# Optimization experiments

Hardware: AMD Instinct MI355X
Metric: run time of the kernel (lower is better)

Reference implementation:

```python
import jax, jax.numpy as jnp
import numpy as np

B, N, K, H = 8, 1024, 16, 4
EMB = 1024

def lrelu(x):
    return jnp.where(x >= 0, x, 0.2 * x)

def bn(x, g, b):
    # eval-mode BatchNorm with running_mean=0, running_var=1
    inv = 1.0 / np.sqrt(1.0 + 1e-5)
    shape = (1, -1) + (1,) * (x.ndim - 2)
    return x * (g * inv).reshape(shape) + b.reshape(shape)

def conv1x1(x, w):
    # 1x1 conv == channel matmul; x: (B,C,...), w: (O,C)
    return jnp.einsum('bc...,oc->bo...', x, w)

def knn_idx(x, k):
    # x: (B,C,N); negative squared pairwise distance, top-k largest = nearest
    inner = -2.0 * jnp.einsum('bcn,bcm->bnm', x, x)
    xx = jnp.sum(x * x, axis=1)                      # (B,N)
    pd = -xx[:, :, None] - inner - xx[:, None, :]
    return jax.lax.top_k(pd, k)[1]                   # (B,N,k)

def graph_feature(x, idx):
    b = x.shape[0]
    xt = jnp.transpose(x, (0, 2, 1))                 # (B,N,C)
    nbr = xt[jnp.arange(b)[:, None, None], idx]      # (B,N,K,C) gather
    ctr = jnp.broadcast_to(xt[:, :, None, :], nbr.shape)
    f = jnp.concatenate([nbr - ctr, ctr], axis=-1)   # (B,N,K,2C)
    return jnp.transpose(f, (0, 3, 1, 2))            # (B,2C,N,K)

def mak(x, y, w0, g0, b0, wm, gm, bm, w1, go, bo, ws, gs, bs, out_ch, in_ch):
    # Multi-head adaptive kernel: generate per-point (out,in,H) weights from y, apply to x
    Bc, _, Nc, Kc = x.shape
    y = lrelu(bn(conv1x1(y, w0), g0, b0))
    y = lrelu(bn(conv1x1(y, wm), gm, bm))
    y = conv1x1(y, w1)                               # (B, out*in*H, N, K)
    w = jnp.transpose(y, (0, 2, 3, 1)).reshape(Bc, Nc, Kc, out_ch, in_ch, H)
    xt = jnp.transpose(x, (0, 2, 3, 1))              # (B,N,K,in)
    # per-head matmul then sum over heads == single einsum over i and h
    out = jnp.einsum('bnkoih,bnki->bonk', w, xt)
    out = bn(out, go, bo)
    idt = bn(conv1x1(x, ws), gs, bs)                 # shortcut (in != out)
    return lrelu(out + idt)


def setup_inputs() -> dict:
    ks = jax.random.split(jax.random.key(0), 48)
    it = iter(range(48))
    def nrm(shape, fan):
        return jax.random.normal(ks[next(it)], shape, jnp.float32) / np.sqrt(fan)
    def gam(c):
        return jax.random.uniform(ks[next(it)], (c,), jnp.float32, 0.5, 1.5)
    def bet(c):
        return 0.1 * jax.random.normal(ks[next(it)], (c,), jnp.float32)
    d = {}
    d['x'] = jax.random.normal(ks[next(it)], (B, 3, N), jnp.float32)
    def mak_params(p, feat_c):
        d[p + '_w0'] = nrm((64, feat_c), feat_c); d[p + '_g0'] = gam(64); d[p + '_b0'] = bet(64)
        d[p + '_wm'] = nrm((64, 64), 64); d[p + '_gm'] = gam(64); d[p + '_bm'] = bet(64)
        d[p + '_w1'] = nrm((64 * 6 * H, 64), 64)
        d[p + '_go'] = gam(64); d[p + '_bo'] = bet(64)
        d[p + '_ws'] = nrm((64, 6), 6); d[p + '_gs'] = gam(64); d[p + '_bs'] = bet(64)
    mak_params('m1', 6)
    mak_params('m2', 128)
    d['w3'] = nrm((128, 128), 128); d['g3'] = gam(128); d['b3'] = bet(128)
    d['w4'] = nrm((256, 256), 256); d['g4'] = gam(256); d['b4'] = bet(256)
    d['w5'] = nrm((EMB, 512), 512); d['g5'] = gam(EMB); d['b5'] = bet(EMB)
    d['wl1'] = nrm((512, 2 * EMB), 2 * EMB); d['bn4_g'] = gam(512); d['bn4_b'] = bet(512)
    d['wl2'] = nrm((256, 512), 512); d['bl2'] = bet(256); d['bn5_g'] = gam(256); d['bn5_b'] = bet(256)
    d['wl3'] = nrm((49, 256), 256); d['bl3'] = bet(49)
    return d


def reference(x, m1_w0, m1_g0, m1_b0, m1_wm, m1_gm, m1_bm, m1_w1, m1_go, m1_bo, m1_ws, m1_gs, m1_bs, m2_w0, m2_g0, m2_b0, m2_wm, m2_gm, m2_bm, m2_w1, m2_go, m2_bo, m2_ws, m2_gs, m2_bs, w3, g3, b3, w4, g4, b4, w5, g5, b5, wl1, bn4_g, bn4_b, wl2, bl2, bn5_g, bn5_b, wl3, bl3):
    idx = knn_idx(x, K)                              # common_idx from points
    geo = graph_feature(x, idx)                      # (B,6,N,K); feat_x == geo_x at stage 1
    h = mak(geo, geo, m1_w0, m1_g0, m1_b0, m1_wm, m1_gm, m1_bm, m1_w1, m1_go, m1_bo, m1_ws, m1_gs, m1_bs, 64, 6)
    x1 = h.max(axis=-1)                              # (B,64,N)
    feat2 = graph_feature(x1, idx)                   # (B,128,N,K)
    h = mak(geo, feat2, m2_w0, m2_g0, m2_b0, m2_wm, m2_gm, m2_bm, m2_w1, m2_go, m2_bo, m2_ws, m2_gs, m2_bs, 64, 6)
    x2 = h.max(axis=-1)                              # (B,64,N)
    x3 = lrelu(bn(conv1x1(graph_feature(x2, idx), w3), g3, b3)).max(axis=-1)   # (B,128,N)
    x4 = lrelu(bn(conv1x1(graph_feature(x3, idx), w4), g4, b4)).max(axis=-1)   # (B,256,N)
    xc = jnp.concatenate([x1, x2, x3, x4], axis=1)   # (B,512,N)
    x5 = lrelu(bn(conv1x1(xc, w5), g5, b5))          # (B,EMB,N)
    xp = jnp.concatenate([x5.max(axis=-1), x5.mean(axis=-1)], axis=1)  # (B,2*EMB)
    xf = lrelu(bn(xp @ wl1.T, bn4_g, bn4_b))
    xf = lrelu(bn(xf @ wl2.T + bl2, bn5_g, bn5_b))
    return xf @ wl3.T + bl3                           # (B,49)
```

## Files before the change

### kernel.cpp

```cpp
#include <hip/hip_runtime.h>
#include <math.h>

#define BB 8
#define NN 1024
#define KK 16
#define NKP (NN*KK)
#define BN_INV 0.99999500003749981f

typedef unsigned short u16;
typedef __attribute__((ext_vector_type(8))) short short8;
typedef __attribute__((ext_vector_type(4))) float f32x4;

#define MFMA16(a,b,c) __builtin_amdgcn_mfma_f32_16x16x32_bf16(a,b,c,0,0,0)

__device__ __forceinline__ float lrelu(float v) { return v >= 0.f ? v : 0.2f * v; }

__device__ __forceinline__ u16 f2bf(float f) {
  union { float f; unsigned u; } v; v.f = f;
  unsigned r = v.u + 0x7fff + ((v.u >> 16) & 1);
  return (u16)(r >> 16);
}
__device__ __forceinline__ float bf2f(u16 s) {
  union { unsigned u; float f; } v; v.u = ((unsigned)s) << 16;
  return v.f;
}

constexpr size_t OFF_IDX   = 0;
constexpr size_t OFF_X1P   = 524288;
constexpr size_t OFF_X2P   = 1572864;
constexpr size_t OFF_X3P   = 2621440;
constexpr size_t OFF_X4P   = 4718592;
constexpr size_t OFF_PMAX  = 8912896;
constexpr size_t OFF_PSUM  = 9437184;
constexpr size_t OFF_XP    = 9961472;
constexpr size_t OFF_XF1   = 10027008;
constexpr size_t OFF_XF2   = 10043392;
constexpr size_t OFF_M1W0  = 10051584;
constexpr size_t OFF_M1WM  = 10055680;
constexpr size_t OFF_M1W1S = 10063872;
constexpr size_t OFF_M2W0  = 10117120;
constexpr size_t OFF_M2WM  = 10133504;
constexpr size_t OFF_M2W1S = 10141696;
constexpr size_t OFF_W3S   = 10194944;
constexpr size_t OFF_W4S   = 10227712;
constexpr size_t OFF_W5    = 10358784;
constexpr size_t OFF_WL1T  = 11407360;
constexpr size_t OFF_WL2T  = 15601664;
constexpr size_t OFF_WL3T  = 16125952;
constexpr size_t OFF_UV3   = 16177152;
constexpr size_t OFF_UV4   = 20371456;

struct SSeg { const float* w; const float* g; u16* dst; int O; int C; int cpl2; int ch; int stk; int start; };
struct SArgs { SSeg seg[7]; int total; };

__global__ __launch_bounds__(256) void prep_scale_bf16(SArgs a) {
  const int tid = blockIdx.x * 256 + threadIdx.x;
  if (tid >= a.total) return;
  int s = 0;
  #pragma unroll
  for (int i = 1; i < 7; ++i) if (tid >= a.seg[i].start) s = i;
  const SSeg sg = a.seg[s];
  const int e = tid - sg.start;
  const int o2 = e >> sg.cpl2;
  const int c = e & ((1 << sg.cpl2) - 1);
  float v = 0.f;
  if (sg.stk) {
    const int half = sg.O >> 1;
    const int o = o2 & (half - 1);
    const int CIN = 2 * sg.C;
    const float wd = sg.w[o * CIN + c];
    v = (o2 < half) ? wd : (sg.w[o * CIN + sg.C + c] - wd);
    v *= sg.g[o] * BN_INV;
  } else if (c < sg.C) {
    v = sg.w[o2 * sg.C + c];
    if (sg.ch && c >= sg.ch) v -= sg.w[o2 * sg.C + c - sg.ch];
    v *= sg.g[o2] * BN_INV;
  }
  sg.dst[(size_t)(c >> 5) * (sg.O * 32) + o2 * 32 + (c & 31)] = f2bf(v);
}

__global__ __launch_bounds__(256) void prep_w1s_bf16(
    const float* __restrict__ w1a, const float* __restrict__ wsa,
    const float* __restrict__ goa, const float* __restrict__ gsa,
    const float* __restrict__ w1b, const float* __restrict__ wsb,
    const float* __restrict__ gob, const float* __restrict__ gsb,
    u16* __restrict__ dsta, u16* __restrict__ dstb) {
  const int tid = blockIdx.x * 256 + threadIdx.x;
  if (tid >= 64 * 416) return;
  const float* w1 = blockIdx.y ? w1b : w1a;
  const float* wsm = blockIdx.y ? wsb : wsa;
  const float* go = blockIdx.y ? gob : goa;
  const float* gs = blockIdx.y ? gsb : gsa;
  u16* dst = blockIdx.y ? dstb : dsta;
  const int o = tid / 416, ci = tid - o * 416;
  float v = 0.f;
  if (ci < 384) {
    const int ii = ci >> 6, ch = ci & 63;
    const int base = (o * 24 + ii * 4) * 64 + ch;
    v = go[o] * BN_INV * (w1[base] + w1[base + 64] + w1[base + 128] + w1[base + 192]);
  } else if (ci < 390) {
    v = gs[o] * BN_INV * wsm[o * 6 + (ci - 384)];
  }
  dst[(size_t)(ci >> 5) * 2048 + o * 32 + (ci & 31)] = f2bf(v);
}

struct TSeg { const float* w; const float* g; float* dst; int O; int C; int start; };
struct TArgs3 { TSeg seg[3]; int total; };

__global__ __launch_bounds__(256) void prep_transpose_f32(TArgs3 a) {
  const int tid = blockIdx.x * 256 + threadIdx.x;
  if (tid >= a.total) return;
  int s = 0;
  #pragma unroll
  for (int i = 1; i < 3; ++i) if (tid >= a.seg[i].start) s = i;
  const TSeg sg = a.seg[s];
  const int e = tid - sg.start;
  const int c = e / sg.O;
  const int o = e - c * sg.O;
  float v = sg.w[o * sg.C + c];
  if (sg.g) v *= sg.g[o] * BN_INV;
  sg.dst[e] = v;
}

__global__ __launch_bounds__(256) void knn_kernel(const float* __restrict__ x, int* __restrict__ idxout) {
  const int wid  = (blockIdx.x * blockDim.x + threadIdx.x) >> 6;
  const int lane = threadIdx.x & 63;
  const int b = wid >> 10;
  const int n = wid & (NN - 1);
  const float* xb = x + b * 3 * NN;
  const float x0n = xb[n], x1n = xb[NN + n], x2n = xb[2 * NN + n];
  const float xxn = x0n * x0n + x1n * x1n + x2n * x2n;
  float pd[16];
  #pragma unroll
  for (int j = 0; j < 16; ++j) {
    const int m = j * 64 + lane;
    const float x0 = xb[m], x1 = xb[NN + m], x2 = xb[2 * NN + m];
    const float dot = x0n * x0 + x1n * x1 + x2n * x2;
    const float xxm = x0 * x0 + x1 * x1 + x2 * x2;
    pd[j] = 2.f * dot - xxn - xxm;
  }
  for (int r = 0; r < 16; ++r) {
    float bv = pd[0]; int bj = 0;
    #pragma unroll
    for (int j = 1; j < 16; ++j) if (pd[j] > bv) { bv = pd[j]; bj = j; }
    int bm = bj * 64 + lane;
    #pragma unroll
    for (int off = 32; off > 0; off >>= 1) {
      const float ov = __shfl_down(bv, off);
      const int   om = __shfl_down(bm, off);
      if (ov > bv || (ov == bv && om < bm)) { bv = ov; bm = om; }
    }
    bm = __shfl(bm, 0);
    if (lane == 0) idxout[wid * KK + r] = bm;
    const int  cj   = bm >> 6;
    const bool mine = (bm & 63) == lane;
    #pragma unroll
    for (int j = 0; j < 16; ++j) if (mine && j == cj) pd[j] = -INFINITY;
  }
}

__device__ __forceinline__ short8 bfrag64(const u16* T, int pl, int quad, int c0) {
  const int pos = ((c0 >> 3) + quad) ^ (pl & 7);
  return *(const short8*)(T + pl * 64 + pos * 8);
}
__device__ __forceinline__ void writeD64(u16* T, int pl, int quad, const f32x4 a,
                                         const float* __restrict__ bias, int obase) {
  union { ushort4 v; u16 s[4]; } pk;
  #pragma unroll
  for (int r = 0; r < 4; ++r) pk.s[r] = f2bf(lrelu(a[r] + bias[obase + quad * 4 + r]));
  const int g = (obase + quad * 4) >> 3;
  const int pos = g ^ (pl & 7);
  *(ushort4*)(T + pl * 64 + pos * 8 + (quad & 1) * 4) = pk.v;
}

template<int CIN_Y>
__global__ __launch_bounds__(256) void mak_mfma(
    const float* __restrict__ x, const int* __restrict__ idxb, const u16* __restrict__ srcp,
    const u16* __restrict__ w0b, const float* __restrict__ b0v,
    const u16* __restrict__ wmb, const float* __restrict__ bmv,
    const u16* __restrict__ w1s, const float* __restrict__ bov, const float* __restrict__ bsv,
    u16* __restrict__ Xoutp) {
  __shared__ __align__(16) u16 Y0s[64 * 64];
  __shared__ __align__(16) u16 YMs[64 * 64];

  const int t = threadIdx.x;
  const int b = blockIdx.z;
  const int p0 = blockIdx.x * 64;
  const int w = t >> 6, l = t & 63;
  const int quad = l >> 4, l15 = l & 15;
  const int pl = w * 16 + l15;
  const int cq8 = quad * 8;
  const int nvtx = blockIdx.x * 4 + w;

  const int nbr = idxb[b * NKP + p0 + pl] & (NN - 1);

  const float* xb = x + b * 3 * NN;
  float ge[6];
  #pragma unroll
  for (int i = 0; i < 3; ++i) {
    const float fc = xb[i * NN + nvtx];
    ge[i]     = xb[i * NN + nbr] - fc;
    ge[3 + i] = fc;
  }
  union { short8 v; u16 s[8]; } bg;
  bg.v = (short8)(short)0;
  if (quad == 0) {
    #pragma unroll
    for (int j = 0; j < 6; ++j) bg.s[j] = f2bf(ge[j]);
  }

  f32x4 acc[4];
  #pragma unroll
  for (int i = 0; i < 4; ++i) acc[i] = (f32x4)0.f;

  if constexpr (CIN_Y == 6) {
    #pragma unroll
    for (int at = 0; at < 4; ++at) {
      const short8 af = *(const short8*)(w0b + (size_t)(at * 16 + l15) * 32 + cq8);
      acc[at] = MFMA16(af, bg.v, acc[at]);
    }
  } else {
    short8 bf[4];
    #pragma unroll
    for (int k = 0; k < 2; ++k)
      bf[k] = *(const short8*)(srcp + (size_t)(b * NN + nbr) * 64 + k * 32 + cq8);
    #pragma unroll
    for (int k = 2; k < 4; ++k)
      bf[k] = *(const short8*)(srcp + (size_t)(b * NN + nvtx) * 64 + (k - 2) * 32 + cq8);
    #pragma unroll
    for (int k = 0; k < 4; ++k) {
      #pragma unroll
      for (int at = 0; at < 4; ++at) {
        const short8 af = *(const short8*)(w0b + (size_t)(k * 64 + at * 16 + l15) * 32 + cq8);
        acc[at] = MFMA16(af, bf[k], acc[at]);
      }
    }
  }
  #pragma unroll
  for (int at = 0; at < 4; ++at) writeD64(Y0s, pl, quad, acc[at], b0v, at * 16);

  #pragma unroll
  for (int i = 0; i < 4; ++i) acc[i] = (f32x4)0.f;
  #pragma unroll
  for (int kc = 0; kc < 2; ++kc) {
    const short8 bf = bfrag64(Y0s, pl, quad, kc * 32);
    #pragma unroll
    for (int at = 0; at < 4; ++at) {
      const short8 af = *(const short8*)(wmb + (size_t)(kc * 64 + at * 16 + l15) * 32 + cq8);
      acc[at] = MFMA16(af, bf, acc[at]);
    }
  }
  #pragma unroll
  for (int at = 0; at < 4; ++at) writeD64(YMs, pl, quad, acc[at], bmv, at * 16);

  short8 bf3[2];
  #pragma unroll
  for (int kc = 0; kc < 2; ++kc) bf3[kc] = bfrag64(YMs, pl, quad, kc * 32);

  #pragma unroll
  for (int i = 0; i < 4; ++i) acc[i] = (f32x4)0.f;
  #pragma unroll
  for (int ii = 0; ii < 6; ++ii) {
    f32x4 tacc[4];
    #pragma unroll
    for (int i = 0; i < 4; ++i) tacc[i] = (f32x4)0.f;
    #pragma unroll
    for (int kc = 0; kc < 2; ++kc) {
      #pragma unroll
      for (int at = 0; at < 4; ++at) {
        const short8 af = *(const short8*)(w1s + (size_t)((ii * 2 + kc) * 64 + at * 16 + l15) * 32 + cq8);
        tacc[at] = MFMA16(af, bf3[kc], tacc[at]);
      }
    }
    const float g = ge[ii];
    #pragma unroll
    for (int at = 0; at < 4; ++at) acc[at] += g * tacc[at];
  }
  #pragma unroll
  for (int at = 0; at < 4; ++at) {
    const short8 af = *(const short8*)(w1s + (size_t)(12 * 64 + at * 16 + l15) * 32 + cq8);
    acc[at] = MFMA16(af, bg.v, acc[at]);
  }

  u16* orow = Xoutp + (size_t)(b * NN + nvtx) * 64;
  #pragma unroll
  for (int at = 0; at < 4; ++at) {
    union { ushort4 v; u16 s[4]; } pk;
    #pragma unroll
    for (int r = 0; r < 4; ++r) {
      const int o = at * 16 + quad * 4 + r;
      float v = lrelu(acc[at][r] + bov[o] + bsv[o]);
      v = fmaxf(v, __shfl_xor(v, 1));
      v = fmaxf(v, __shfl_xor(v, 2));
      v = fmaxf(v, __shfl_xor(v, 4));
      v = fmaxf(v, __shfl_xor(v, 8));
      pk.s[r] = f2bf(v);
    }
    if (l15 == 0) *(ushort4*)(orow + at * 16 + quad * 4) = pk.v;
  }
}

template<int CH, int COUT2>
__global__ __launch_bounds__(256) void dense_uv(
    const u16* __restrict__ srcp, const u16* __restrict__ w2,
    const float* __restrict__ bias, u16* __restrict__ UV) {
  constexpr int COUT = COUT2 / 2;
  constexpr int NCH = CH / 32;
  const int t = threadIdx.x;
  const int b = blockIdx.z;
  const int n0 = blockIdx.x * 64;
  const int w = t >> 6, l = t & 63;
  const int quad = l >> 4, l15 = l & 15;
  const int cq8 = quad * 8;
  const int ow0 = blockIdx.y * 256 + w * 64;

  f32x4 acc[4][4];
  #pragma unroll
  for (int i = 0; i < 4; ++i)
    #pragma unroll
    for (int j = 0; j < 4; ++j) acc[i][j] = (f32x4)0.f;

  #pragma unroll
  for (int k = 0; k < NCH; ++k) {
    short8 bfr[4];
    #pragma unroll
    for (int pg = 0; pg < 4; ++pg) {
      const int n = n0 + pg * 16 + l15;
      bfr[pg] = *(const short8*)(srcp + (size_t)(b * NN + n) * CH + k * 32 + cq8);
    }
    #pragma unroll
    for (int at = 0; at < 4; ++at) {
      const short8 af = *(const short8*)(w2 + ((size_t)(k * COUT2 + ow0 + at * 16 + l15)) * 32 + cq8);
      #pragma unroll
      for (int pg = 0; pg < 4; ++pg) acc[at][pg] = MFMA16(af, bfr[pg], acc[at][pg]);
    }
  }

  #pragma unroll
  for (int at = 0; at < 4; ++at) {
    const int o0 = ow0 + at * 16 + quad * 4;
    const bool isv = (o0 >= COUT);
    float bb[4];
    #pragma unroll
    for (int r = 0; r < 4; ++r) bb[r] = isv ? bias[o0 + r - COUT] : 0.f;
    #pragma unroll
    for (int pg = 0; pg < 4; ++pg) {
      const int n = n0 + pg * 16 + l15;
      union { ushort4 v; u16 s[4]; } pk;
      #pragma unroll
      for (int r = 0; r < 4; ++r) pk.s[r] = f2bf(acc[at][pg][r] + bb[r]);
      *(ushort4*)(UV + (size_t)(b * NN + n) * COUT2 + o0) = pk.v;
    }
  }
}

__device__ __forceinline__ float4 ubf4(ushort4 q) {
  float4 f;
  f.x = bf2f(q.x); f.y = bf2f(q.y); f.z = bf2f(q.z); f.w = bf2f(q.w);
  return f;
}

template<int COUT>
__global__ __launch_bounds__(256) void gather_max(
    const u16* __restrict__ UV, const int* __restrict__ idxb,
    u16* __restrict__ Xoutp) {
  constexpr int CG = COUT / 4;
  const int tid = blockIdx.x * 256 + threadIdx.x;
  const int cg = tid & (CG - 1);
  const int P = tid / CG;
  const int b = P >> 10;
  const int n = P & (NN - 1);

  const float4 vv = ubf4(*(const ushort4*)(UV + (size_t)P * (2 * COUT) + COUT + 4 * cg));
  const int4* ip = (const int4*)(idxb + (size_t)b * NKP + n * 16);
  float4 m = {-INFINITY, -INFINITY, -INFINITY, -INFINITY};
  #pragma unroll
  for (int kq = 0; kq < 4; ++kq) {
    const int4 iv = ip[kq];
    const int mr[4] = { iv.x & (NN - 1), iv.y & (NN - 1), iv.z & (NN - 1), iv.w & (NN - 1) };
    ushort4 uq[4];
    #pragma unroll
    for (int j = 0; j < 4; ++j)
      uq[j] = *(const ushort4*)(UV + (size_t)(b * NN + mr[j]) * (2 * COUT) + 4 * cg);
    #pragma unroll
    for (int j = 0; j < 4; ++j) {
      const float4 uu = ubf4(uq[j]);
      float4 s;
      s.x = uu.x + vv.x; s.y = uu.y + vv.y; s.z = uu.z + vv.z; s.w = uu.w + vv.w;
      m.x = fmaxf(m.x, fmaxf(s.x, 0.2f * s.x));
      m.y = fmaxf(m.y, fmaxf(s.y, 0.2f * s.y));
      m.z = fmaxf(m.z, fmaxf(s.z, 0.2f * s.z));
      m.w = fmaxf(m.w, fmaxf(s.w, 0.2f * s.w));
    }
  }
  union { ushort4 v; u16 s[4]; } pk;
  pk.s[0] = f2bf(m.x); pk.s[1] = f2bf(m.y); pk.s[2] = f2bf(m.z); pk.s[3] = f2bf(m.w);
  *(ushort4*)(Xoutp + (size_t)P * COUT + 4 * cg) = pk.v;
}

__global__ __launch_bounds__(256) void conv5_mfma(
    const u16* __restrict__ X1P, const u16* __restrict__ X2P,
    const u16* __restrict__ X3P, const u16* __restrict__ X4P,
    const u16* __restrict__ w5b, const float* __restrict__ b5,
    float* __restrict__ PMAX, float* __restrict__ PSUM) {
  const int t = threadIdx.x;
  const int b = blockIdx.z;
  const int n0 = blockIdx.x * 64;
  const int w = t >> 6, l = t & 63;
  const int quad = l >> 4, l15 = l & 15;
  const int cq8 = quad * 8;
  const int ow0 = blockIdx.y * 256 + w * 64;

  f32x4 acc[4][4];
  #pragma unroll
  for (int i = 0; i < 4; ++i)
    #pragma unroll
    for (int j = 0; j < 4; ++j) acc[i][j] = (f32x4)0.f;

  #pragma unroll 4
  for (int k = 0; k < 16; ++k) {
    const int c = k * 32 + cq8;
    short8 bfr[4];
    #pragma unroll
    for (int pg = 0; pg < 4; ++pg) {
      const int n = n0 + pg * 16 + l15;
      const u16* src; int cc;
      if (c < 64)       { src = X1P + (size_t)(b * NN + n) * 64;  cc = c; }
      else if (c < 128) { src = X2P + (size_t)(b * NN + n) * 64;  cc = c - 64; }
      else if (c < 256) { src = X3P + (size_t)(b * NN + n) * 128; cc = c - 128; }
      else              { src = X4P + (size_t)(b * NN + n) * 256; cc = c - 256; }
      bfr[pg] = *(const short8*)(src + cc);
    }
    #pragma unroll
    for (int at = 0; at < 4; ++at) {
      const short8 af = *(const short8*)(w5b + ((size_t)(k * 1024 + ow0 + at * 16 + l15)) * 32 + cq8);
      #pragma unroll
      for (int pg = 0; pg < 4; ++pg) acc[at][pg] = MFMA16(af, bfr[pg], acc[at][pg]);
    }
  }

  #pragma unroll
  for (int at = 0; at < 4; ++at) {
    f32x4 pmx, psm;
    #pragma unroll
    for (int r = 0; r < 4; ++r) {
      const float bb = b5[ow0 + at * 16 + quad * 4 + r];
      float m = -INFINITY, s = 0.f;
      #pragma unroll
      for (int pg = 0; pg < 4; ++pg) {
        const float v = lrelu(acc[at][pg][r] + bb);
        m = fmaxf(m, v); s += v;
      }
      #pragma unroll
      for (int msk = 1; msk < 16; msk <<= 1) {
        m = fmaxf(m, __shfl_xor(m, msk));
        s += __shfl_xor(s, msk);
      }
      pmx[r] = m; psm[r] = s;
    }
    if (l15 == 0) {
      float* dm = PMAX + (size_t)(b * 16 + blockIdx.x) * 1024 + ow0 + at * 16 + quad * 4;
      float* ds = PSUM + (size_t)(b * 16 + blockIdx.x) * 1024 + ow0 + at * 16 + quad * 4;
      *(f32x4*)dm = pmx;
      *(f32x4*)ds = psm;
    }
  }
}

__global__ __launch_bounds__(256) void reduce5(const float* __restrict__ PMAX, const float* __restrict__ PSUM,
                                               float* __restrict__ XPg) {
  const int tid = blockIdx.x * 256 + threadIdx.x;
  const int b = tid >> 10, o = tid & 1023;
  float m = -INFINITY, s = 0.f;
  for (int pt = 0; pt < 16; ++pt) {
    m = fmaxf(m, PMAX[(size_t)(b * 16 + pt) * 1024 + o]);
    s += PSUM[(size_t)(b * 16 + pt) * 1024 + o];
  }
  XPg[b * 2048 + o] = m;
  XPg[b * 2048 + 1024 + o] = s * (1.f / 1024.f);
}

__global__ __launch_bounds__(256) void fc1_kernel(const float* __restrict__ XPg, const float* __restrict__ wl1t,
                                                  const float* __restrict__ bn4_b, float* __restrict__ XF1) {
  __shared__ float red[64 * 5];
  const int t = threadIdx.x;
  const int b = blockIdx.y;
  const int o = blockIdx.x * 64 + (t & 63);
  const int cq = t >> 6;
  const float* xp = XPg + b * 2048;
  float acc = 0.f;
  for (int c = cq * 512; c < cq * 512 + 512; ++c) acc = fmaf(wl1t[c * 512 + o], xp[c], acc);
  red[(t & 63) * 5 + cq] = acc;
  __syncthreads();
  if (t < 64) {
    const int oo = blockIdx.x * 64 + t;
    const float v = red[t * 5] + red[t * 5 + 1] + red[t * 5 + 2] + red[t * 5 + 3] + bn4_b[oo];
    XF1[b * 512 + oo] = lrelu(v);
  }
}

__global__ __launch_bounds__(256) void fc2_kernel(const float* __restrict__ XF1, const float* __restrict__ wl2t,
                                                  const float* __restrict__ bl2, const float* __restrict__ bn5_g,
                                                  const float* __restrict__ bn5_b, float* __restrict__ XF2) {
  __shared__ float red[64 * 5];
  const int t = threadIdx.x;
  const int b = blockIdx.y;
  const int o = blockIdx.x * 64 + (t & 63);
  const int cq = t >> 6;
  const float* xf = XF1 + b * 512;
  float acc = 0.f;
  for (int c = cq * 128; c < cq * 128 + 128; ++c) acc = fmaf(wl2t[c * 256 + o], xf[c], acc);
  red[(t & 63) * 5 + cq] = acc;
  __syncthreads();
  if (t < 64) {
    const int oo = blockIdx.x * 64 + t;
    const float bias = bl2[oo] * (bn5_g[oo] * BN_INV) + bn5_b[oo];
    const float v = red[t * 5] + red[t * 5 + 1] + red[t * 5 + 2] + red[t * 5 + 3] + bias;
    XF2[b * 256 + oo] = lrelu(v);
  }
}

__global__ __launch_bounds__(256) void fc3_kernel(const float* __restrict__ XF2, const float* __restrict__ wl3t,
                                                  const float* __restrict__ bl3, float* __restrict__ out) {
  __shared__ float red[64 * 5];
  const int t = threadIdx.x;
  const int b = blockIdx.y;
  const int ol = t & 63;
  const int cq = t >> 6;
  const float* xf = XF2 + b * 256;
  float acc = 0.f;
  if (ol < 49) for (int c = cq * 64; c < cq * 64 + 64; ++c) acc = fmaf(wl3t[c * 49 + ol], xf[c], acc);
  red[ol * 5 + cq] = acc;
  __syncthreads();
  if (t < 49) out[b * 49 + t] = red[t * 5] + red[t * 5 + 1] + red[t * 5 + 2] + red[t * 5 + 3] + bl3[t];
}

extern "C" void kernel_launch(void* const* d_in, const int* in_sizes, int n_in,
                              void* d_out, int out_size, void* d_ws, size_t ws_size,
                              hipStream_t stream) {
  (void)in_sizes; (void)n_in; (void)out_size; (void)ws_size;
  const float* x     = (const float*)d_in[0];
  const float* m1_w0 = (const float*)d_in[1];
  const float* m1_g0 = (const float*)d_in[2];
  const float* m1_b0 = (const float*)d_in[3];
  const float* m1_wm = (const float*)d_in[4];
  const float* m1_gm = (const float*)d_in[5];
  const float* m1_bm = (const float*)d_in[6];
  const float* m1_w1 = (const float*)d_in[7];
  const float* m1_go = (const float*)d_in[8];
  const float* m1_bo = (const float*)d_in[9];
  const float* m1_ws = (const float*)d_in[10];
  const float* m1_gs = (const float*)d_in[11];
  const float* m1_bs = (const float*)d_in[12];
  const float* m2_w0 = (const float*)d_in[13];
  const float* m2_g0 = (const float*)d_in[14];
  const float* m2_b0 = (const float*)d_in[15];
  const float* m2_wm = (const float*)d_in[16];
  const float* m2_gm = (const float*)d_in[17];
  const float* m2_bm = (const float*)d_in[18];
  const float* m2_w1 = (const float*)d_in[19];
  const float* m2_go = (const float*)d_in[20];
  const float* m2_bo = (const float*)d_in[21];
  const float* m2_ws = (const float*)d_in[22];
  const float* m2_gs = (const float*)d_in[23];
  const float* m2_bs = (const float*)d_in[24];
  const float* w3    = (const float*)d_in[25];
  const float* g3    = (const float*)d_in[26];
  const float* b3    = (const float*)d_in[27];
  const float* w4    = (const float*)d_in[28];
  const float* g4    = (const float*)d_in[29];
  const float* b4    = (const float*)d_in[30];
  const float* w5    = (const float*)d_in[31];
  const float* g5    = (const float*)d_in[32];
  const float* b5    = (const float*)d_in[33];
  const float* wl1   = (const float*)d_in[34];
  const float* bn4_g = (const float*)d_in[35];
  const float* bn4_b = (const float*)d_in[36];
  const float* wl2   = (const float*)d_in[37];
  const float* bl2   = (const float*)d_in[38];
  const float* bn5_g = (const float*)d_in[39];
  const float* bn5_b = (const float*)d_in[40];
  const float* wl3   = (const float*)d_in[41];
  const float* bl3   = (const float*)d_in[42];

  char* wsb = (char*)d_ws;
  int*  IDX  = (int*)(wsb + OFF_IDX);
  u16*  X1P  = (u16*)(wsb + OFF_X1P);
  u16*  X2P  = (u16*)(wsb + OFF_X2P);
  u16*  X3P  = (u16*)(wsb + OFF_X3P);
  u16*  X4P  = (u16*)(wsb + OFF_X4P);
  float* PMAX = (float*)(wsb + OFF_PMAX);
  float* PSUM = (float*)(wsb + OFF_PSUM);
  float* XPg  = (float*)(wsb + OFF_XP);
  float* XF1  = (float*)(wsb + OFF_XF1);
  float* XF2  = (float*)(wsb + OFF_XF2);
  u16*  M1W0 = (u16*)(wsb + OFF_M1W0);
  u16*  M1WM = (u16*)(wsb + OFF_M1WM);
  u16*  M1W1S = (u16*)(wsb + OFF_M1W1S);
  u16*  M2W0 = (u16*)(wsb + OFF_M2W0);
  u16*  M2WM = (u16*)(wsb + OFF_M2WM);
  u16*  M2W1S = (u16*)(wsb + OFF_M2W1S);
  u16*  W3S  = (u16*)(wsb + OFF_W3S);
  u16*  W4S  = (u16*)(wsb + OFF_W4S);
  u16*  W5B  = (u16*)(wsb + OFF_W5);
  float* WL1T = (float*)(wsb + OFF_WL1T);
  float* WL2T = (float*)(wsb + OFF_WL2T);
  float* WL3T = (float*)(wsb + OFF_WL3T);
  u16*  UV3  = (u16*)(wsb + OFF_UV3);
  u16*  UV4  = (u16*)(wsb + OFF_UV4);

  SArgs sa; int st = 0;
  auto sset = [&](int i, const float* w, const float* g, u16* dst, int O, int C, int cpl2, int ch, int stk) {
    sa.seg[i].w = w; sa.seg[i].g = g; sa.seg[i].dst = dst; sa.seg[i].O = O; sa.seg[i].C = C;
    sa.seg[i].cpl2 = cpl2; sa.seg[i].ch = ch; sa.seg[i].stk = stk; sa.seg[i].start = st;
    st += O << cpl2;
  };
  sset(0, m1_w0, m1_g0, M1W0, 64, 6, 5, 0, 0);
  sset(1, m1_wm, m1_gm, M1WM, 64, 64, 6, 0, 0);
  sset(2, m2_w0, m2_g0, M2W0, 64, 128, 7, 64, 0);
  sset(3, m2_wm, m2_gm, M2WM, 64, 64, 6, 0, 0);
  sset(4, w3, g3, W3S, 256, 64, 6, 0, 1);
  sset(5, w4, g4, W4S, 512, 128, 7, 0, 1);
  sset(6, w5, g5, W5B, 1024, 512, 9, 0, 0);
  sa.total = st;

  TArgs3 ta; int tt = 0;
  auto tset = [&](int i, const float* w, const float* g, float* dst, int O, int C) {
    ta.seg[i].w = w; ta.seg[i].g = g; ta.seg[i].dst = dst; ta.seg[i].O = O; ta.seg[i].C = C;
    ta.seg[i].start = tt; tt += O * C;
  };
  tset(0, wl1, bn4_g, WL1T, 512, 2048);
  tset(1, wl2, bn5_g, WL2T, 256, 512);
  tset(2, wl3, nullptr, WL3T, 49, 256);
  ta.total = tt;

  hipLaunchKernelGGL(prep_scale_bf16, dim3((sa.total + 255) / 256), dim3(256), 0, stream, sa);
  hipLaunchKernelGGL(prep_w1s_bf16, dim3(104, 2), dim3(256), 0, stream,
                     m1_w1, m1_ws, m1_go, m1_gs, m2_w1, m2_ws, m2_go, m2_gs, M1W1S, M2W1S);
  hipLaunchKernelGGL(prep_transpose_f32, dim3((ta.total + 255) / 256), dim3(256), 0, stream, ta);

  hipLaunchKernelGGL(knn_kernel, dim3(2048), dim3(256), 0, stream, x, IDX);

  hipLaunchKernelGGL((mak_mfma<6>), dim3(256, 1, BB), dim3(256), 0, stream,
                     x, IDX, (const u16*)nullptr, M1W0, m1_b0, M1WM, m1_bm, M1W1S, m1_bo, m1_bs, X1P);
  hipLaunchKernelGGL((mak_mfma<128>), dim3(256, 1, BB), dim3(256), 0, stream,
                     x, IDX, X1P, M2W0, m2_b0, M2WM, m2_bm, M2W1S, m2_bo, m2_bs, X2P);

  hipLaunchKernelGGL((dense_uv<64, 256>), dim3(16, 1, BB), dim3(256), 0, stream, X2P, W3S, b3, UV3);
  hipLaunchKernelGGL((gather_max<128>), dim3(1024), dim3(256), 0, stream, UV3, IDX, X3P);

  hipLaunchKernelGGL((dense_uv<128, 512>), dim3(16, 2, BB), dim3(256), 0, stream, X3P, W4S, b4, UV4);
  hipLaunchKernelGGL((gather_max<256>), dim3(2048), dim3(256), 0, stream, UV4, IDX, X4P);

  hipLaunchKernelGGL(conv5_mfma, dim3(16, 4, BB), dim3(256), 0, stream,
                     X1P, X2P, X3P, X4P, W5B, b5, PMAX, PSUM);
  hipLaunchKernelGGL(reduce5, dim3(32), dim3(256), 0, stream, PMAX, PSUM, XPg);

  hipLaunchKernelGGL(fc1_kernel, dim3(8, BB), dim3(256), 0, stream, XPg, WL1T, bn4_b, XF1);
  hipLaunchKernelGGL(fc2_kernel, dim3(4, BB), dim3(256), 0, stream, XF1, WL2T, bl2, bn5_g, bn5_b, XF2);
  hipLaunchKernelGGL(fc3_kernel, dim3(1, BB), dim3(256), 0, stream, XF2, WL3T, bl3, (float*)d_out);
}
```

Baseline: 386.8 us.

## Factor MAK first conv into per-point U/V terms and split edge build

The first 1x1 conv of each MAK block acts on concatenated [nbr-ctr, ctr] features, so it is rewritten as per-point projections U (neighbor) and V (center) computed once per point. A separate edge-build kernel gathers U[nbr]+V[n], applies lrelu and stores the edge activations and geometric features to global memory. The remaining MFMA kernel then reads these instead of recomputing the first conv per edge. This removes redundant per-edge matmul work, especially for the 128-channel stage 2, but adds extra kernel launches and a large round trip of edge tensors through global memory.

```diff
diff --git a/kernel.cpp b/kernel.cpp
--- a/kernel.cpp
+++ b/kernel.cpp
@@ -29,16 +29,17 @@
 constexpr size_t OFF_X1P   = 524288;
 constexpr size_t OFF_X2P   = 1572864;
 constexpr size_t OFF_X3P   = 2621440;
+constexpr size_t OFF_MUV   = 2621440;
 constexpr size_t OFF_X4P   = 4718592;
+constexpr size_t OFF_GEO   = 4718592;
 constexpr size_t OFF_PMAX  = 8912896;
 constexpr size_t OFF_PSUM  = 9437184;
 constexpr size_t OFF_XP    = 9961472;
 constexpr size_t OFF_XF1   = 10027008;
 constexpr size_t OFF_XF2   = 10043392;
-constexpr size_t OFF_M1W0  = 10051584;
 constexpr size_t OFF_M1WM  = 10055680;
 constexpr size_t OFF_M1W1S = 10063872;
-constexpr size_t OFF_M2W0  = 10117120;
+constexpr size_t OFF_M2W0S = 10117120;
 constexpr size_t OFF_M2WM  = 10133504;
 constexpr size_t OFF_M2W1S = 10141696;
 constexpr size_t OFF_W3S   = 10194944;
@@ -48,17 +49,18 @@
 constexpr size_t OFF_WL2T  = 15601664;
 constexpr size_t OFF_WL3T  = 16125952;
 constexpr size_t OFF_UV3   = 16177152;
+constexpr size_t OFF_EY0   = 16177152;
 constexpr size_t OFF_UV4   = 20371456;
 
 struct SSeg { const float* w; const float* g; u16* dst; int O; int C; int cpl2; int ch; int stk; int start; };
-struct SArgs { SSeg seg[7]; int total; };
+struct SArgs { SSeg seg[6]; int total; };
 
 __global__ __launch_bounds__(256) void prep_scale_bf16(SArgs a) {
   const int tid = blockIdx.x * 256 + threadIdx.x;
   if (tid >= a.total) return;
   int s = 0;
   #pragma unroll
-  for (int i = 1; i < 7; ++i) if (tid >= a.seg[i].start) s = i;
+  for (int i = 1; i < 6; ++i) if (tid >= a.seg[i].start) s = i;
   const SSeg sg = a.seg[s];
   const int e = tid - sg.start;
   const int o2 = e >> sg.cpl2;
@@ -173,77 +175,90 @@
   *(ushort4*)(T + pl * 64 + pos * 8 + (quad & 1) * 4) = pk.v;
 }
 
-template<int CIN_Y>
-__global__ __launch_bounds__(256) void mak_mfma(
-    const float* __restrict__ x, const int* __restrict__ idxb, const u16* __restrict__ srcp,
-    const u16* __restrict__ w0b, const float* __restrict__ b0v,
+__global__ __launch_bounds__(256) void mak1_uv(
+    const float* __restrict__ x, const float* __restrict__ w0,
+    const float* __restrict__ g0, const float* __restrict__ b0,
+    u16* __restrict__ MUV) {
+  const int tid = blockIdx.x * 256 + threadIdx.x;
+  if (tid >= BB * NN * 64) return;
+  const int o = tid & 63;
+  const int p = tid >> 6;
+  const int b = p >> 10, n = p & (NN - 1);
+  const float* xb = x + b * 3 * NN;
+  const float gg = g0[o] * BN_INV;
+  float u = 0.f, v = 0.f;
+  #pragma unroll
+  for (int i = 0; i < 3; ++i) {
+    const float wd = w0[o * 6 + i];
+    const float wc = w0[o * 6 + 3 + i];
+    const float c = xb[i * NN + n];
+    u += wd * c;
+    v += (wc - wd) * c;
+  }
+  MUV[(size_t)p * 128 + o]      = f2bf(gg * u);
+  MUV[(size_t)p * 128 + 64 + o] = f2bf(gg * v + b0[o]);
+}
+
+__global__ __launch_bounds__(256) void mak_edge_build(
+    const float* __restrict__ x, const int* __restrict__ idxb,
+    const u16* __restrict__ MUV, u16* __restrict__ EY0,
+    u16* __restrict__ GEO, int writeGeo) {
+  const int tid = blockIdx.x * 256 + threadIdx.x;
+  const int cg = tid & 7;
+  const int e = tid >> 3;
+  const int b = e >> 14;
+  const int nk = e & 16383;
+  const int n = nk >> 4;
+  const int nbr = idxb[e] & (NN - 1);
+  union { uint4 q; u16 s[8]; } uu, vv, rr;
+  uu.q = *(const uint4*)(MUV + (size_t)(b * NN + nbr) * 128 + cg * 8);
+  vv.q = *(const uint4*)(MUV + (size_t)(b * NN + n) * 128 + 64 + cg * 8);
+  #pragma unroll
+  for (int j = 0; j < 8; ++j) rr.s[j] = f2bf(lrelu(bf2f(uu.s[j]) + bf2f(vv.s[j])));
+  *(uint4*)(EY0 + (size_t)e * 64 + cg * 8) = rr.q;
+  if (writeGeo && cg == 0) {
+    const float* xb = x + b * 3 * NN;
+    union { uint4 q; u16 s[8]; } g;
+    #pragma unroll
+    for (int i = 0; i < 3; ++i) {
+      const float fc = xb[i * NN + n];
+      g.s[i]     = f2bf(xb[i * NN + nbr] - fc);
+      g.s[3 + i] = f2bf(fc);
+    }
+    g.s[6] = 0; g.s[7] = 0;
+    *(uint4*)(GEO + (size_t)e * 8) = g.q;
+  }
+}
+
+__global__ __launch_bounds__(256) void mak23_mfma(
+    const u16* __restrict__ EY0, const u16* __restrict__ GEO,
     const u16* __restrict__ wmb, const float* __restrict__ bmv,
     const u16* __restrict__ w1s, const float* __restrict__ bov, const float* __restrict__ bsv,
     u16* __restrict__ Xoutp) {
-  __shared__ __align__(16) u16 Y0s[64 * 64];
   __shared__ __align__(16) u16 YMs[64 * 64];
 
   const int t = threadIdx.x;
   const int b = blockIdx.z;
-  const int p0 = blockIdx.x * 64;
   const int w = t >> 6, l = t & 63;
   const int quad = l >> 4, l15 = l & 15;
   const int pl = w * 16 + l15;
   const int cq8 = quad * 8;
   const int nvtx = blockIdx.x * 4 + w;
-
-  const int nbr = idxb[b * NKP + p0 + pl] & (NN - 1);
-
-  const float* xb = x + b * 3 * NN;
+  const size_t eL = ((size_t)(b * NN + nvtx)) * 16 + l15;
+
+  union { short8 v; u16 s[8]; } gq;
+  gq.v = *(const short8*)(GEO + eL * 8);
   float ge[6];
   #pragma unroll
-  for (int i = 0; i < 3; ++i) {
-    const float fc = xb[i * NN + nvtx];
-    ge[i]     = xb[i * NN + nbr] - fc;
-    ge[3 + i] = fc;
-  }
-  union { short8 v; u16 s[8]; } bg;
-  bg.v = (short8)(short)0;
-  if (quad == 0) {
-    #pragma unroll
-    for (int j = 0; j < 6; ++j) bg.s[j] = f2bf(ge[j]);
-  }
+  for (int ii = 0; ii < 6; ++ii) ge[ii] = bf2f(gq.s[ii]);
+  const short8 bgv = (quad == 0) ? gq.v : (short8)(short)0;
 
   f32x4 acc[4];
   #pragma unroll
   for (int i = 0; i < 4; ++i) acc[i] = (f32x4)0.f;
-
-  if constexpr (CIN_Y == 6) {
-    #pragma unroll
-    for (int at = 0; at < 4; ++at) {
-      const short8 af = *(const short8*)(w0b + (size_t)(at * 16 + l15) * 32 + cq8);
-      acc[at] = MFMA16(af, bg.v, acc[at]);
-    }
-  } else {
-    short8 bf[4];
-    #pragma unroll
-    for (int k = 0; k < 2; ++k)
-      bf[k] = *(const short8*)(srcp + (size_t)(b * NN + nbr) * 64 + k * 32 + cq8);
-    #pragma unroll
-    for (int k = 2; k < 4; ++k)
-      bf[k] = *(const short8*)(srcp + (size_t)(b * NN + nvtx) * 64 + (k - 2) * 32 + cq8);
-    #pragma unroll
-    for (int k = 0; k < 4; ++k) {
-      #pragma unroll
-      for (int at = 0; at < 4; ++at) {
-        const short8 af = *(const short8*)(w0b + (size_t)(k * 64 + at * 16 + l15) * 32 + cq8);
-        acc[at] = MFMA16(af, bf[k], acc[at]);
-      }
-    }
-  }
-  #pragma unroll
-  for (int at = 0; at < 4; ++at) writeD64(Y0s, pl, quad, acc[at], b0v, at * 16);
-
-  #pragma unroll
-  for (int i = 0; i < 4; ++i) acc[i] = (f32x4)0.f;
   #pragma unroll
   for (int kc = 0; kc < 2; ++kc) {
-    const short8 bf = bfrag64(Y0s, pl, quad, kc * 32);
+    const short8 bf = *(const short8*)(EY0 + eL * 64 + kc * 32 + cq8);
     #pragma unroll
     for (int at = 0; at < 4; ++at) {
       const short8 af = *(const short8*)(wmb + (size_t)(kc * 64 + at * 16 + l15) * 32 + cq8);
@@ -279,7 +294,7 @@
   #pragma unroll
   for (int at = 0; at < 4; ++at) {
     const short8 af = *(const short8*)(w1s + (size_t)(12 * 64 + at * 16 + l15) * 32 + cq8);
-    acc[at] = MFMA16(af, bg.v, acc[at]);
+    acc[at] = MFMA16(af, bgv, acc[at]);
   }
 
   u16* orow = Xoutp + (size_t)(b * NN + nvtx) * 64;
@@ -308,11 +323,12 @@
   constexpr int NCH = CH / 32;
   const int t = threadIdx.x;
   const int b = blockIdx.z;
-  const int n0 = blockIdx.x * 64;
   const int w = t >> 6, l = t & 63;
   const int quad = l >> 4, l15 = l & 15;
   const int cq8 = quad * 8;
-  const int ow0 = blockIdx.y * 256 + w * 64;
+  int n0, ow0;
+  if constexpr (COUT2 >= 256) { n0 = blockIdx.x * 64; ow0 = blockIdx.y * 256 + w * 64; }
+  else { n0 = blockIdx.x * 128 + (w >> 1) * 64; ow0 = (w & 1) * 64; }
 
   f32x4 acc[4][4];
   #pragma unroll
@@ -589,15 +605,17 @@
   u16*  X2P  = (u16*)(wsb + OFF_X2P);
   u16*  X3P  = (u16*)(wsb + OFF_X3P);
   u16*  X4P  = (u16*)(wsb + OFF_X4P);
+  u16*  MUV  = (u16*)(wsb + OFF_MUV);
+  u16*  GEO  = (u16*)(wsb + OFF_GEO);
+  u16*  EY0  = (u16*)(wsb + OFF_EY0);
   float* PMAX = (float*)(wsb + OFF_PMAX);
   float* PSUM = (float*)(wsb + OFF_PSUM);
   float* XPg  = (float*)(wsb + OFF_XP);
   float* XF1  = (float*)(wsb + OFF_XF1);
   float* XF2  = (float*)(wsb + OFF_XF2);
-  u16*  M1W0 = (u16*)(wsb + OFF_M1W0);
   u16*  M1WM = (u16*)(wsb + OFF_M1WM);
   u16*  M1W1S = (u16*)(wsb + OFF_M1W1S);
-  u16*  M2W0 = (u16*)(wsb + OFF_M2W0);
+  u16*  M2W0S = (u16*)(wsb + OFF_M2W0S);
   u16*  M2WM = (u16*)(wsb + OFF_M2WM);
   u16*  M2W1S = (u16*)(wsb + OFF_M2W1S);
   u16*  W3S  = (u16*)(wsb + OFF_W3S);
@@ -615,13 +633,12 @@
     sa.seg[i].cpl2 = cpl2; sa.seg[i].ch = ch; sa.seg[i].stk = stk; sa.seg[i].start = st;
     st += O << cpl2;
   };
-  sset(0, m1_w0, m1_g0, M1W0, 64, 6, 5, 0, 0);
-  sset(1, m1_wm, m1_gm, M1WM, 64, 64, 6, 0, 0);
-  sset(2, m2_w0, m2_g0, M2W0, 64, 128, 7, 64, 0);
-  sset(3, m2_wm, m2_gm, M2WM, 64, 64, 6, 0, 0);
-  sset(4, w3, g3, W3S, 256, 64, 6, 0, 1);
-  sset(5, w4, g4, W4S, 512, 128, 7, 0, 1);
-  sset(6, w5, g5, W5B, 1024, 512, 9, 0, 0);
+  sset(0, m1_wm, m1_gm, M1WM, 64, 64, 6, 0, 0);
+  sset(1, m2_w0, m2_g0, M2W0S, 128, 64, 6, 0, 1);
+  sset(2, m2_wm, m2_gm, M2WM, 64, 64, 6, 0, 0);
+  sset(3, w3, g3, W3S, 256, 64, 6, 0, 1);
+  sset(4, w4, g4, W4S, 512, 128, 7, 0, 1);
+  sset(5, w5, g5, W5B, 1024, 512, 9, 0, 0);
   sa.total = st;
 
   TArgs3 ta; int tt = 0;
@@ -641,14 +658,19 @@
 
   hipLaunchKernelGGL(knn_kernel, dim3(2048), dim3(256), 0, stream, x, IDX);
 
-  hipLaunchKernelGGL((mak_mfma<6>), dim3(256, 1, BB), dim3(256), 0, stream,
-                     x, IDX, (const u16*)nullptr, M1W0, m1_b0, M1WM, m1_bm, M1W1S, m1_bo, m1_bs, X1P);
-  hipLaunchKernelGGL((mak_mfma<128>), dim3(256, 1, BB), dim3(256), 0, stream,
-                     x, IDX, X1P, M2W0, m2_b0, M2WM, m2_bm, M2W1S, m2_bo, m2_bs, X2P);
+  hipLaunchKernelGGL(mak1_uv, dim3((BB * NN * 64 + 255) / 256), dim3(256), 0, stream,
+                     x, m1_w0, m1_g0, m1_b0, MUV);
+  hipLaunchKernelGGL(mak_edge_build, dim3(4096), dim3(256), 0, stream, x, IDX, MUV, EY0, GEO, 1);
+  hipLaunchKernelGGL(mak23_mfma, dim3(256, 1, BB), dim3(256), 0, stream,
+                     EY0, GEO, M1WM, m1_bm, M1W1S, m1_bo, m1_bs, X1P);
+
+  hipLaunchKernelGGL((dense_uv<64, 128>), dim3(8, 1, BB), dim3(256), 0, stream, X1P, M2W0S, m2_b0, MUV);
+  hipLaunchKernelGGL(mak_edge_build, dim3(4096), dim3(256), 0, stream, x, IDX, MUV, EY0, GEO, 0);
+  hipLaunchKernelGGL(mak23_mfma, dim3(256, 1, BB), dim3(256), 0, stream,
+                     EY0, GEO, M2WM, m2_bm, M2W1S, m2_bo, m2_bs, X2P);
 
   hipLaunchKernelGGL((dense_uv<64, 256>), dim3(16, 1, BB), dim3(256), 0, stream, X2P, W3S, b3, UV3);
   hipLaunchKernelGGL((gather_max<128>), dim3(1024), dim3(256), 0, stream, UV3, IDX, X3P);
-
   hipLaunchKernelGGL((dense_uv<128, 512>), dim3(16, 2, BB), dim3(256), 0, stream, X3P, W4S, b4, UV4);
   hipLaunchKernelGGL((gather_max<256>), dim3(2048), dim3(256), 0, stream, UV4, IDX, X4P);
 
```

Result: slower. 409.0 us (+5.8%).
